# Performance work log

Measured on AMD Instinct MI355X. Metric: run time of the kernel, lower is better.

The kernel has to match this reference:

```python
import jax, jax.numpy as jnp
import numpy as np

BATCH, SEQ, FEAT, NUM_BINS = 64, 1024, 512, 32


def setup_inputs() -> dict:
    key = jax.random.key(0)
    k1, k2 = jax.random.split(key)
    features = jax.random.normal(k1, (BATCH, SEQ, FEAT), dtype=jnp.float32)
    # buffer: randn(input_dim, num_bins) / sqrt(input_dim)
    random_projection = jax.random.normal(k2, (FEAT, NUM_BINS), dtype=jnp.float32) / np.sqrt(FEAT)
    return {"features": features, "random_projection": random_projection}


def reference(features, random_projection):
    batch, seq, feat = features.shape
    x = features.reshape(-1, feat)  # [N, feat]
    N = x.shape[0]

    # RunningMeanStd.update from fresh state (mean=0, var=1, count=1e-4)
    eps_count = 1e-4
    batch_mean = x.mean(axis=0)
    batch_var = jnp.var(x, axis=0, ddof=1)  # torch.var is unbiased by default
    tot = eps_count + N
    delta = batch_mean  # - 0
    mean = delta * N / tot
    M2 = 1.0 * eps_count + batch_var * N + (delta ** 2) * eps_count * N / tot
    var = M2 / tot
    sigma = jnp.sqrt(var + 1e-8)

    normalized = (x - mean) / sigma
    projected = normalized @ random_projection  # [N, num_bins]
    bits = (projected > 0).astype(jnp.int64)
    pow2 = jnp.left_shift(jnp.int64(1), jnp.arange(NUM_BINS, dtype=jnp.int64))
    keys = (bits * pow2).sum(axis=-1)  # [N], values < 2^32

    # env_indices=None path: env = arange(N) % batch
    env = jnp.arange(N, dtype=jnp.int64) % batch
    combined = jnp.left_shift(env, 32) | keys  # unique (env, key) id

    # running occurrence count of each (env, key) in sample order i=0..N-1
    order = jnp.argsort(combined, stable=True)  # stable: preserves sample order within group
    s = combined[order]
    idx = jnp.arange(N, dtype=jnp.int64)
    is_start = jnp.concatenate([jnp.ones((1,), bool), s[1:] != s[:-1]])
    seg_start = jax.lax.cummax(jnp.where(is_start, idx, 0))
    occ = idx - seg_start + 1  # 1-based occurrence within group
    counts = jnp.zeros((N,), jnp.int64).at[order].set(occ)

    rewards = 1.0 / jnp.sqrt(counts.astype(features.dtype))
    return rewards.reshape(batch, seq, 1)
```

## Files before the change

kernel.cpp:

```cpp
#include <hip/hip_runtime.h>

using u16 = unsigned short;
using u64 = unsigned long long;
typedef short s16x8 __attribute__((ext_vector_type(8)));
typedef unsigned short u16x4 __attribute__((ext_vector_type(4)));
typedef float f32x4 __attribute__((ext_vector_type(4)));

constexpr int BATCH = 64, SEQ = 1024, FEAT = 512, NBINS = 32;
constexpr int N = BATCH * SEQ;
constexpr int TAB = 131072;
constexpr unsigned TABMASK = TAB - 1;
constexpr u64 EMPTY = ~0ull;
constexpr double FXSCALE = 67108864.0;
constexpr int NSHADOW = 64;


constexpr size_t OFF_KEYS = 0;
constexpr size_t OFF_HEAD = 1048576;
constexpr size_t OFF_CNT = 1572864;
constexpr size_t OFF_SHAD = 2097152;
constexpr size_t OFF_QD = 2621440;
constexpr size_t OFF_CD = 2752512;
constexpr size_t OFF_CF = 2818304;
constexpr size_t OFF_SLOT = 2818432;
constexpr size_t OFF_NEXT = 3080576;
constexpr size_t OFF_QFRAG = 3342720;

__device__ inline u16 f2bf(float f) {
  unsigned u = __builtin_bit_cast(unsigned, f);
  u += 0x7FFFu + ((u >> 16) & 1u);
  return (u16)(u >> 16);
}
__device__ inline float bf2f(u16 h) {
  return __builtin_bit_cast(float, (unsigned)h << 16);
}

__global__ __launch_bounds__(256, 4) void colstats_kernel(
    const float4* __restrict__ xv, u64* __restrict__ shad) {
  const int t = threadIdx.x;
  const int L = blockIdx.x * 256 + t;
  double s0 = 0, s1 = 0, s2 = 0, s3 = 0, q0 = 0, q1 = 0, q2 = 0, q3 = 0;
  for (int mm = 0; mm < 32; mm += 8) {
    float4 v[8];
#pragma unroll
    for (int u = 0; u < 8; u++) v[u] = xv[L + (mm + u) * 262144];
#pragma unroll
    for (int u = 0; u < 8; u++) {
      double a = (double)v[u].x, b = (double)v[u].y;
      double c = (double)v[u].z, d = (double)v[u].w;
      s0 += a; s1 += b; s2 += c; s3 += d;
      q0 += a * a; q1 += b * b; q2 += c * c; q3 += d * d;
    }
  }
  __shared__ double red[256 * 8];
  red[t * 8 + 0] = s0; red[t * 8 + 1] = s1; red[t * 8 + 2] = s2; red[t * 8 + 3] = s3;
  red[t * 8 + 4] = q0; red[t * 8 + 5] = q1; red[t * 8 + 6] = q2; red[t * 8 + 7] = q3;
  __syncthreads();
  if (t < 128) {
    double v[8];
#pragma unroll
    for (int u = 0; u < 8; u++) v[u] = red[t * 8 + u] + red[(t + 128) * 8 + u];
    const int c0 = 4 * t;
    u64* sh = shad + (size_t)(blockIdx.x & (NSHADOW - 1)) * 1024;
#pragma unroll
    for (int u = 0; u < 4; u++) {
      long long a = (long long)llrint(v[u] * FXSCALE);
      long long b = (long long)llrint(v[4 + u] * FXSCALE);
      atomicAdd(&sh[c0 + u], (u64)a);
      atomicAdd(&sh[512 + c0 + u], (u64)b);
    }
  }
}

__global__ __launch_bounds__(512) void finalize_kernel(
    const float* __restrict__ P,
    const u64* __restrict__ shad,
    double* __restrict__ Qd, u16* __restrict__ qfrag,
    double* __restrict__ cd, float* __restrict__ cf) {
  __shared__ double meanArr[FEAT];
  __shared__ double invArr[FEAT];
  __shared__ double part[16][NBINS];
  const int t = threadIdx.x;
  long long isum = 0, isumsq = 0;
  for (int sh = 0; sh < NSHADOW; sh++) {
    isum += (long long)shad[sh * 1024 + t];
    isumsq += (long long)shad[sh * 1024 + 512 + t];
  }
  const double Nd = (double)N;
  const double tot = 1e-4 + Nd;
  double s = (double)isum * (1.0 / FXSCALE);
  double ss = (double)isumsq * (1.0 / FXSCALE);
  double bm = s / Nd;
  double bv = (ss - s * s / Nd) / (Nd - 1.0);
  double mean = bm * Nd / tot;
  double M2 = 1e-4 + bv * Nd + bm * bm * 1e-4 * Nd / tot;
  double var = M2 / tot;
  double inv = 1.0 / sqrt(var + 1e-8);
  meanArr[t] = mean;
  invArr[t] = inv;
  const int ch = t >> 7, ks = (t >> 5) & 3, kg = (t >> 3) & 3, jlo = t & 7;
#pragma unroll
  for (int j = 0; j < NBINS; j++) {
    double qd = (double)P[t * NBINS + j] * inv;
    Qd[t * NBINS + j] = qd;
    const u16 qh = f2bf((float)qd);
    const u16 ql = f2bf((float)(qd - (double)bf2f(qh)));
    const int lane = (j & 15) | (kg << 4);
    const int bt = j >> 4;
    const size_t base =
        (size_t)(((((ch * 4 + ks) * 2 + bt) * 2) * 64 + lane) * 8 + jlo);
    qfrag[base] = qh;
    qfrag[base + 512] = ql;
  }
  __syncthreads();
  {
    const int j = t & 31, g = t >> 5;
    double p = 0.0;
    for (int f = g * 32; f < g * 32 + 32; f++) {
      double qd = (double)P[f * NBINS + j] * invArr[f];
      p += meanArr[f] * qd;
    }
    part[g][j] = p;
  }
  __syncthreads();
  if (t < NBINS) {
    double c = 0.0;
    for (int g = 0; g < 16; g++) c += part[g][t];
    cd[t] = c;
    cf[t] = (float)c;
  }
}

constexpr float TAU = 2.5e-3f;
__global__ __launch_bounds__(256, 3) void project_kernel(
    const float4* __restrict__ xv, const float* __restrict__ feat,
    const u16* __restrict__ qfrag, const float* __restrict__ cf,
    const double* __restrict__ Qd, const double* __restrict__ cd,
    u64* __restrict__ keys_tab, int* __restrict__ head,
    unsigned* __restrict__ cnt, int* __restrict__ slot, int* __restrict__ nxt) {
  __shared__ __align__(16) u16 xh_lds[8192];
  __shared__ __align__(16) u16 xl_lds[8192];
  __shared__ unsigned keyParts[64];
  const int t = threadIdx.x;
  const int rowBase = blockIdx.x * 64;
  const int lane = t & 63;
  const int w = t >> 6;
  if (t < 64) keyParts[t] = 0u;

  f32x4 acc0 = {0.f, 0.f, 0.f, 0.f};
  f32x4 acc1 = {0.f, 0.f, 0.f, 0.f};
  for (int ch = 0; ch < 4; ch++) {
    __syncthreads();
    s16x8 Bh[4][2], Bl[4][2];
#pragma unroll
    for (int ks = 0; ks < 4; ks++)
#pragma unroll
      for (int bt = 0; bt < 2; bt++) {
        const size_t b =
            (size_t)(((((ch * 4 + ks) * 2 + bt) * 2) * 64 + lane) * 8);
        Bh[ks][bt] = *(const s16x8*)&qfrag[b];
        Bl[ks][bt] = *(const s16x8*)&qfrag[b + 512];
      }
#pragma unroll
    for (int kk = 0; kk < 8; kk++) {
      const int vi = t + kk * 256;
      const int r = vi >> 5, f4 = vi & 31;
      float4 v = xv[(size_t)(rowBase + r) * 128 + ch * 32 + f4];
      const int ks = f4 >> 3, kg = (f4 & 7) >> 1, j0 = (f4 & 1) * 4;
      const int lane_ = (r & 15) | (kg << 4);
      const int blk = ((r >> 4) * 4 + ks) * 64 + (lane_ ^ (((lane_ >> 4) & 3) << 1));
      u16x4 hv, lv;
      float xs[4] = {v.x, v.y, v.z, v.w};
#pragma unroll
      for (int c2 = 0; c2 < 4; c2++) {
        const u16 h = f2bf(xs[c2]);
        hv[c2] = h;
        lv[c2] = f2bf(xs[c2] - bf2f(h));
      }
      *(u16x4*)&xh_lds[blk * 8 + j0] = hv;
      *(u16x4*)&xl_lds[blk * 8 + j0] = lv;
    }
    __syncthreads();
#pragma unroll
    for (int ks = 0; ks < 4; ks++) {
      const int rblk = (w * 4 + ks) * 64 + (lane ^ (((lane >> 4) & 3) << 1));
      s16x8 aH = *(const s16x8*)&xh_lds[rblk * 8];
      s16x8 aL = *(const s16x8*)&xl_lds[rblk * 8];
      acc0 = __builtin_amdgcn_mfma_f32_16x16x32_bf16(aH, Bh[ks][0], acc0, 0, 0, 0);
      acc1 = __builtin_amdgcn_mfma_f32_16x16x32_bf16(aH, Bh[ks][1], acc1, 0, 0, 0);
      acc0 = __builtin_amdgcn_mfma_f32_16x16x32_bf16(aL, Bh[ks][0], acc0, 0, 0, 0);
      acc1 = __builtin_amdgcn_mfma_f32_16x16x32_bf16(aL, Bh[ks][1], acc1, 0, 0, 0);
      acc0 = __builtin_amdgcn_mfma_f32_16x16x32_bf16(aH, Bl[ks][0], acc0, 0, 0, 0);
      acc1 = __builtin_amdgcn_mfma_f32_16x16x32_bf16(aH, Bl[ks][1], acc1, 0, 0, 0);
    }
  }
  const int colbin = lane & 15;
  float m0[4], m1[4];
  bool b0[4], b1[4];
  const float c0v = cf[colbin], c1v = cf[16 + colbin];
#pragma unroll
  for (int rg = 0; rg < 4; rg++) {
    m0[rg] = acc0[rg] - c0v;
    m1[rg] = acc1[rg] - c1v;
    b0[rg] = m0[rg] > 0.0f;
    b1[rg] = m1[rg] > 0.0f;
  }
#pragma unroll
  for (int bt = 0; bt < 2; bt++)
#pragma unroll
    for (int rg = 0; rg < 4; rg++) {
      const float mv = (bt == 0) ? m0[rg] : m1[rg];
      u64 mask = __ballot(fabsf(mv) < TAU);
      while (mask) {
        const int L = (int)__builtin_ctzll(mask);
        mask &= mask - 1;
        const int jj = bt * 16 + (L & 15);
        const int row = rowBase + w * 16 + (L >> 4) * 4 + rg;
        const float* xr = feat + (size_t)row * FEAT + lane * 8;
        const double* qp = Qd + (size_t)(lane * 8) * NBINS + jj;
        double p = 0.0;
#pragma unroll
        for (int u = 0; u < 8; u++) p = fma((double)xr[u], qp[u * NBINS], p);
#pragma unroll
        for (int off = 32; off > 0; off >>= 1) p += __shfl_xor(p, off, 64);
        const bool bit = p > cd[jj];
        if (lane == L) {
          if (bt == 0) b0[rg] = bit; else b1[rg] = bit;
        }
      }
    }
#pragma unroll
  for (int rg = 0; rg < 4; rg++) {
    const unsigned mybits = (b0[rg] ? (1u << colbin) : 0u) |
                            (b1[rg] ? (1u << (16 + colbin)) : 0u);
    atomicOr(&keyParts[w * 16 + (lane >> 4) * 4 + rg], mybits);
  }
  __syncthreads();
  if (t < 64) {
    const int i = rowBase + t;
    unsigned key = keyParts[t];
    u64 combined = (u64)key;
    unsigned idx = (unsigned)((combined * 0x9E3779B97F4A7C15ull) >> 47) & TABMASK;
    for (;;) {
      u64 prev = atomicCAS(&keys_tab[idx], EMPTY, combined);
      if (prev == EMPTY || prev == combined) break;
      idx = (idx + 1) & TABMASK;
    }
    slot[i] = (int)idx;
    atomicAdd(&cnt[idx], 1u);
    nxt[i] = atomicExch(&head[idx], i);
  }
}

__global__ __launch_bounds__(256) void count_kernel(
    const int* __restrict__ slot, const int* __restrict__ nxt,
    const int* __restrict__ head, const unsigned* __restrict__ cnt,
    float* __restrict__ out) {
  const int i = blockIdx.x * 256 + threadIdx.x;
  const int sl = slot[i];
  const unsigned c = cnt[sl];
  float r = 1.0f;
  if (c > 1u) {
    int j = head[sl];
    int occ = 1;
    while (j >= 0) {
      occ += (j < i) ? 1 : 0;
      j = nxt[j];
    }
    r = 1.0f / sqrtf((float)occ);
  }
  out[i] = r;
}

extern "C" void kernel_launch(void* const* d_in, const int* in_sizes, int n_in,
                              void* d_out, int out_size, void* d_ws, size_t ws_size,
                              hipStream_t stream) {
  const float4* xv = (const float4*)d_in[0];
  const float* feat = (const float*)d_in[0];
  const float* proj = (const float*)d_in[1];
  float* out = (float*)d_out;
  char* ws = (char*)d_ws;

  u64* keys_tab = (u64*)(ws + OFF_KEYS);
  int* head = (int*)(ws + OFF_HEAD);
  unsigned* cnt = (unsigned*)(ws + OFF_CNT);
  u64* shad = (u64*)(ws + OFF_SHAD);
  double* Qd = (double*)(ws + OFF_QD);
  double* cd = (double*)(ws + OFF_CD);
  float* cf = (float*)(ws + OFF_CF);
  int* slot = (int*)(ws + OFF_SLOT);
  int* nxt = (int*)(ws + OFF_NEXT);
  u16* qfrag = (u16*)(ws + OFF_QFRAG);

  hipMemsetAsync(ws + OFF_KEYS, 0xFF, OFF_CNT - OFF_KEYS, stream);
  hipMemsetAsync(ws + OFF_CNT, 0x00, OFF_QD - OFF_CNT, stream);

  colstats_kernel<<<1024, 256, 0, stream>>>(xv, shad);
  finalize_kernel<<<1, 512, 0, stream>>>(proj, shad, Qd, qfrag, cd, cf);
  project_kernel<<<N / 64, 256, 0, stream>>>(xv, feat, qfrag, cf, Qd, cd,
                                             keys_tab, head, cnt, slot, nxt);
  count_kernel<<<N / 256, 256, 0, stream>>>(slot, nxt, head, cnt, out);
}
```

Measured before the change: 271.6 us.

## Use single fp16 MFMA pass and fold finalize into last colstats block

Replaces the three-pass bf16 split (hi/lo) matrix product with a single fp16 MFMA pass. This removes the low-part LDS buffer and two thirds of the MFMAs. The refinement tolerance TAU is widened to cover the larger fp16 error, so more rows may need the exact fallback. The separate single-block finalize kernel is folded into colstats through a last-block-done atomic counter, which saves a kernel launch and the gap between kernels.

Measured after the change: 440.9 us. 1.62x slower.

```diff
diff --git a/kernel.cpp b/kernel.cpp
--- a/kernel.cpp
+++ b/kernel.cpp
@@ -3,6 +3,7 @@
 using u16 = unsigned short;
 using u64 = unsigned long long;
 typedef short s16x8 __attribute__((ext_vector_type(8)));
+typedef _Float16 f16x8 __attribute__((ext_vector_type(8)));
 typedef unsigned short u16x4 __attribute__((ext_vector_type(4)));
 typedef float f32x4 __attribute__((ext_vector_type(4)));
 
@@ -13,30 +14,34 @@
 constexpr u64 EMPTY = ~0ull;
 constexpr double FXSCALE = 67108864.0;
 constexpr int NSHADOW = 64;
+constexpr int NBLK_A = 1024;
 
 
 constexpr size_t OFF_KEYS = 0;
 constexpr size_t OFF_HEAD = 1048576;
 constexpr size_t OFF_CNT = 1572864;
 constexpr size_t OFF_SHAD = 2097152;
-constexpr size_t OFF_QD = 2621440;
-constexpr size_t OFF_CD = 2752512;
+constexpr size_t OFF_FLAG = 2621440;
+constexpr size_t OFF_QD = 2621504;
+constexpr size_t OFF_CD = 2752576;
 constexpr size_t OFF_CF = 2818304;
 constexpr size_t OFF_SLOT = 2818432;
 constexpr size_t OFF_NEXT = 3080576;
 constexpr size_t OFF_QFRAG = 3342720;
 
-__device__ inline u16 f2bf(float f) {
-  unsigned u = __builtin_bit_cast(unsigned, f);
-  u += 0x7FFFu + ((u >> 16) & 1u);
-  return (u16)(u >> 16);
-}
-__device__ inline float bf2f(u16 h) {
-  return __builtin_bit_cast(float, (unsigned)h << 16);
+__device__ inline u16 f2h(float f) {
+  _Float16 h = (_Float16)f;
+  return __builtin_bit_cast(u16, h);
 }
 
 __global__ __launch_bounds__(256, 4) void colstats_kernel(
-    const float4* __restrict__ xv, u64* __restrict__ shad) {
+    const float4* __restrict__ xv,
+    const float* __restrict__ P,
+    u64* __restrict__ shad, unsigned* __restrict__ flag,
+    double* __restrict__ Qd, u16* __restrict__ qfrag,
+    double* __restrict__ cd, float* __restrict__ cf) {
+  __shared__ double red[256 * 8];
+  __shared__ bool isLast;
   const int t = threadIdx.x;
   const int L = blockIdx.x * 256 + t;
   double s0 = 0, s1 = 0, s2 = 0, s3 = 0, q0 = 0, q1 = 0, q2 = 0, q3 = 0;
@@ -52,7 +57,6 @@
       q0 += a * a; q1 += b * b; q2 += c * c; q3 += d * d;
     }
   }
-  __shared__ double red[256 * 8];
   red[t * 8 + 0] = s0; red[t * 8 + 1] = s1; red[t * 8 + 2] = s2; red[t * 8 + 3] = s3;
   red[t * 8 + 4] = q0; red[t * 8 + 5] = q1; red[t * 8 + 6] = q2; red[t * 8 + 7] = q3;
   __syncthreads();
@@ -70,68 +74,69 @@
       atomicAdd(&sh[512 + c0 + u], (u64)b);
     }
   }
-}
-
-__global__ __launch_bounds__(512) void finalize_kernel(
-    const float* __restrict__ P,
-    const u64* __restrict__ shad,
-    double* __restrict__ Qd, u16* __restrict__ qfrag,
-    double* __restrict__ cd, float* __restrict__ cf) {
-  __shared__ double meanArr[FEAT];
-  __shared__ double invArr[FEAT];
-  __shared__ double part[16][NBINS];
-  const int t = threadIdx.x;
-  long long isum = 0, isumsq = 0;
-  for (int sh = 0; sh < NSHADOW; sh++) {
-    isum += (long long)shad[sh * 1024 + t];
-    isumsq += (long long)shad[sh * 1024 + 512 + t];
-  }
-  const double Nd = (double)N;
-  const double tot = 1e-4 + Nd;
-  double s = (double)isum * (1.0 / FXSCALE);
-  double ss = (double)isumsq * (1.0 / FXSCALE);
-  double bm = s / Nd;
-  double bv = (ss - s * s / Nd) / (Nd - 1.0);
-  double mean = bm * Nd / tot;
-  double M2 = 1e-4 + bv * Nd + bm * bm * 1e-4 * Nd / tot;
-  double var = M2 / tot;
-  double inv = 1.0 / sqrt(var + 1e-8);
-  meanArr[t] = mean;
-  invArr[t] = inv;
-  const int ch = t >> 7, ks = (t >> 5) & 3, kg = (t >> 3) & 3, jlo = t & 7;
-#pragma unroll
-  for (int j = 0; j < NBINS; j++) {
-    double qd = (double)P[t * NBINS + j] * inv;
-    Qd[t * NBINS + j] = qd;
-    const u16 qh = f2bf((float)qd);
-    const u16 ql = f2bf((float)(qd - (double)bf2f(qh)));
-    const int lane = (j & 15) | (kg << 4);
-    const int bt = j >> 4;
-    const size_t base =
-        (size_t)(((((ch * 4 + ks) * 2 + bt) * 2) * 64 + lane) * 8 + jlo);
-    qfrag[base] = qh;
-    qfrag[base + 512] = ql;
-  }
-  __syncthreads();
-  {
-    const int j = t & 31, g = t >> 5;
+  __threadfence();
+  __syncthreads();
+  if (t == 0) isLast = (atomicAdd(flag, 1u) == (unsigned)(NBLK_A - 1));
+  __syncthreads();
+  if (!isLast) return;
+  __threadfence();
+
+  double* meanArr = red;
+  double* invArr = red + 512;
+  double* part = red + 1024;
+#pragma unroll
+  for (int half = 0; half < 2; half++) {
+    const int f = t + half * 256;
+    long long isum = 0, isumsq = 0;
+    for (int sh = 0; sh < NSHADOW; sh++) {
+      isum += (long long)__hip_atomic_load(&shad[sh * 1024 + f],
+                                           __ATOMIC_RELAXED, __HIP_MEMORY_SCOPE_AGENT);
+      isumsq += (long long)__hip_atomic_load(&shad[sh * 1024 + 512 + f],
+                                             __ATOMIC_RELAXED, __HIP_MEMORY_SCOPE_AGENT);
+    }
+    const double Nd = (double)N;
+    const double tot = 1e-4 + Nd;
+    double s = (double)isum * (1.0 / FXSCALE);
+    double ss = (double)isumsq * (1.0 / FXSCALE);
+    double bm = s / Nd;
+    double bv = (ss - s * s / Nd) / (Nd - 1.0);
+    double mean = bm * Nd / tot;
+    double M2 = 1e-4 + bv * Nd + bm * bm * 1e-4 * Nd / tot;
+    double var = M2 / tot;
+    double inv = 1.0 / sqrt(var + 1e-8);
+    meanArr[f] = mean;
+    invArr[f] = inv;
+    const int ch = f >> 7, ks = (f >> 5) & 3, kg = (f >> 3) & 3, jlo = f & 7;
+#pragma unroll
+    for (int j = 0; j < NBINS; j++) {
+      double qd = (double)P[f * NBINS + j] * inv;
+      Qd[f * NBINS + j] = qd;
+      const int lane = (j & 15) | (kg << 4);
+      const int bt = j >> 4;
+      qfrag[(size_t)((((ch * 4 + ks) * 2 + bt) * 64 + lane) * 8 + jlo)] =
+          f2h((float)qd);
+    }
+  }
+  __syncthreads();
+#pragma unroll
+  for (int half = 0; half < 2; half++) {
+    const int tt = t + half * 256;
+    const int j = tt & 31, g = tt >> 5;
     double p = 0.0;
-    for (int f = g * 32; f < g * 32 + 32; f++) {
-      double qd = (double)P[f * NBINS + j] * invArr[f];
-      p += meanArr[f] * qd;
-    }
-    part[g][j] = p;
+    for (int f = g * 32; f < g * 32 + 32; f++)
+      p += meanArr[f] * ((double)P[f * NBINS + j] * invArr[f]);
+    part[g * NBINS + j] = p;
   }
   __syncthreads();
   if (t < NBINS) {
     double c = 0.0;
-    for (int g = 0; g < 16; g++) c += part[g][t];
+    for (int g = 0; g < 16; g++) c += part[g * NBINS + t];
     cd[t] = c;
     cf[t] = (float)c;
   }
 }
 
-constexpr float TAU = 2.5e-3f;
+constexpr float TAU = 4e-3f;
 __global__ __launch_bounds__(256, 3) void project_kernel(
     const float4* __restrict__ xv, const float* __restrict__ feat,
     const u16* __restrict__ qfrag, const float* __restrict__ cf,
@@ -139,7 +144,6 @@
     u64* __restrict__ keys_tab, int* __restrict__ head,
     unsigned* __restrict__ cnt, int* __restrict__ slot, int* __restrict__ nxt) {
   __shared__ __align__(16) u16 xh_lds[8192];
-  __shared__ __align__(16) u16 xl_lds[8192];
   __shared__ unsigned keyParts[64];
   const int t = threadIdx.x;
   const int rowBase = blockIdx.x * 64;
@@ -151,16 +155,12 @@
   f32x4 acc1 = {0.f, 0.f, 0.f, 0.f};
   for (int ch = 0; ch < 4; ch++) {
     __syncthreads();
-    s16x8 Bh[4][2], Bl[4][2];
+    s16x8 B[4][2];
 #pragma unroll
     for (int ks = 0; ks < 4; ks++)
 #pragma unroll
-      for (int bt = 0; bt < 2; bt++) {
-        const size_t b =
-            (size_t)(((((ch * 4 + ks) * 2 + bt) * 2) * 64 + lane) * 8);
-        Bh[ks][bt] = *(const s16x8*)&qfrag[b];
-        Bl[ks][bt] = *(const s16x8*)&qfrag[b + 512];
-      }
+      for (int bt = 0; bt < 2; bt++)
+        B[ks][bt] = *(const s16x8*)&qfrag[(size_t)((((ch * 4 + ks) * 2 + bt) * 64 + lane) * 8)];
 #pragma unroll
     for (int kk = 0; kk < 8; kk++) {
       const int vi = t + kk * 256;
@@ -169,29 +169,19 @@
       const int ks = f4 >> 3, kg = (f4 & 7) >> 1, j0 = (f4 & 1) * 4;
       const int lane_ = (r & 15) | (kg << 4);
       const int blk = ((r >> 4) * 4 + ks) * 64 + (lane_ ^ (((lane_ >> 4) & 3) << 1));
-      u16x4 hv, lv;
-      float xs[4] = {v.x, v.y, v.z, v.w};
-#pragma unroll
-      for (int c2 = 0; c2 < 4; c2++) {
-        const u16 h = f2bf(xs[c2]);
-        hv[c2] = h;
-        lv[c2] = f2bf(xs[c2] - bf2f(h));
-      }
+      u16x4 hv;
+      hv[0] = f2h(v.x); hv[1] = f2h(v.y); hv[2] = f2h(v.z); hv[3] = f2h(v.w);
       *(u16x4*)&xh_lds[blk * 8 + j0] = hv;
-      *(u16x4*)&xl_lds[blk * 8 + j0] = lv;
     }
     __syncthreads();
 #pragma unroll
     for (int ks = 0; ks < 4; ks++) {
       const int rblk = (w * 4 + ks) * 64 + (lane ^ (((lane >> 4) & 3) << 1));
-      s16x8 aH = *(const s16x8*)&xh_lds[rblk * 8];
-      s16x8 aL = *(const s16x8*)&xl_lds[rblk * 8];
-      acc0 = __builtin_amdgcn_mfma_f32_16x16x32_bf16(aH, Bh[ks][0], acc0, 0, 0, 0);
-      acc1 = __builtin_amdgcn_mfma_f32_16x16x32_bf16(aH, Bh[ks][1], acc1, 0, 0, 0);
-      acc0 = __builtin_amdgcn_mfma_f32_16x16x32_bf16(aL, Bh[ks][0], acc0, 0, 0, 0);
-      acc1 = __builtin_amdgcn_mfma_f32_16x16x32_bf16(aL, Bh[ks][1], acc1, 0, 0, 0);
-      acc0 = __builtin_amdgcn_mfma_f32_16x16x32_bf16(aH, Bl[ks][0], acc0, 0, 0, 0);
-      acc1 = __builtin_amdgcn_mfma_f32_16x16x32_bf16(aH, Bl[ks][1], acc1, 0, 0, 0);
+      f16x8 a = __builtin_bit_cast(f16x8, *(const s16x8*)&xh_lds[rblk * 8]);
+      acc0 = __builtin_amdgcn_mfma_f32_16x16x32_f16(
+          a, __builtin_bit_cast(f16x8, B[ks][0]), acc0, 0, 0, 0);
+      acc1 = __builtin_amdgcn_mfma_f32_16x16x32_f16(
+          a, __builtin_bit_cast(f16x8, B[ks][1]), acc1, 0, 0, 0);
     }
   }
   const int colbin = lane & 15;
@@ -285,6 +275,7 @@
   int* head = (int*)(ws + OFF_HEAD);
   unsigned* cnt = (unsigned*)(ws + OFF_CNT);
   u64* shad = (u64*)(ws + OFF_SHAD);
+  unsigned* flag = (unsigned*)(ws + OFF_FLAG);
   double* Qd = (double*)(ws + OFF_QD);
   double* cd = (double*)(ws + OFF_CD);
   float* cf = (float*)(ws + OFF_CF);
@@ -292,11 +283,11 @@
   int* nxt = (int*)(ws + OFF_NEXT);
   u16* qfrag = (u16*)(ws + OFF_QFRAG);
 
-  hipMemsetAsync(ws + OFF_KEYS, 0xFF, OFF_CNT - OFF_KEYS, stream);
-  hipMemsetAsync(ws + OFF_CNT, 0x00, OFF_QD - OFF_CNT, stream);
-
-  colstats_kernel<<<1024, 256, 0, stream>>>(xv, shad);
-  finalize_kernel<<<1, 512, 0, stream>>>(proj, shad, Qd, qfrag, cd, cf);
+  (void)hipMemsetAsync(ws + OFF_KEYS, 0xFF, OFF_CNT - OFF_KEYS, stream);
+  (void)hipMemsetAsync(ws + OFF_CNT, 0x00, OFF_QD - OFF_CNT, stream);
+
+  colstats_kernel<<<NBLK_A, 256, 0, stream>>>(xv, proj, shad, flag, Qd, qfrag,
+                                              cd, cf);
   project_kernel<<<N / 64, 256, 0, stream>>>(xv, feat, qfrag, cf, Qd, cd,
                                              keys_tab, head, cnt, slot, nxt);
   count_kernel<<<N / 256, 256, 0, stream>>>(slot, nxt, head, cnt, out);
```
